# Kernel tuning notes

Measured on AMD Instinct MI355X. Metric: run time of the kernel, lower is better.

Reference implementation:

```python
import jax, jax.numpy as jnp
import numpy as np

IN_FEATURES = 512
NUM_TREES = 512
DEPTH = 5
NLEAF = 2 ** DEPTH
RESPONSE_DIM = 1
BATCH = 2048


def make_path_map():
    # OBLIVIOUS_map from DeTree.InitPathWay: nodes[j] = j (oblivious tree),
    # index 2*node + bit into the flattened [depth, 2] choice tensor.
    path = []
    for no in range(NLEAF):
        b = no
        for j in range(DEPTH):
            path.append(2 * j + (b % 2))
            b //= 2
    return np.asarray(path, dtype=np.int32)  # [NLEAF * DEPTH]


def setup_inputs() -> dict:
    key = jax.random.key(0)
    k1, k2, k3, k4, k5 = jax.random.split(key, 5)
    x = jax.random.normal(k1, (BATCH, IN_FEATURES), dtype=jnp.float32)
    # nn.init.uniform_ on [in_features, num_trees * depth]
    feat_attention = jax.random.uniform(k2, (IN_FEATURES, NUM_TREES * DEPTH), dtype=jnp.float32)
    feature_thresholds = jax.random.normal(k3, (NUM_TREES, DEPTH), dtype=jnp.float32)
    log_temperatures = jax.random.normal(k4, (NUM_TREES, DEPTH), dtype=jnp.float32) * 0.1
    response = jax.random.normal(k5, (NUM_TREES, RESPONSE_DIM, NLEAF), dtype=jnp.float32)
    path_map = jnp.asarray(make_path_map())
    return {"x": x, "feat_attention": feat_attention,
            "feature_thresholds": feature_thresholds,
            "log_temperatures": log_temperatures,
            "response": response, "path_map": path_map}


def reference(x, feat_attention, feature_thresholds, log_temperatures, response, path_map):
    B, F = x.shape
    n, d = feature_thresholds.shape
    # feature gating: softmax over the feature axis (dim=0)
    choice_weight = jax.nn.softmax(feat_attention, axis=0).reshape(F, n, d)
    feature_values = jnp.einsum('bf,fnd->bnd', x, choice_weight)  # [B, n, d]
    # temperature-scaled split logits
    tl = (feature_values - feature_thresholds) * jnp.exp(-log_temperatures)
    logits = jnp.stack([-tl, tl], axis=-1)  # [B, n, d, 2]
    # sparsemoid binary gate
    choice = jnp.clip(0.5 * logits + 0.5, 0.0, 1.0)
    # route through tree paths: gather per-leaf path gates, product along depth
    gate = choice.reshape(B, n, d * 2)[:, :, path_map].reshape(B, n, -1, d)
    bins_prob = jnp.prod(gate, axis=-1)  # [B, n, nLeaf]
    out = jnp.einsum('bnl,ncl->bnc', bins_prob, response)  # [B, n, response_dim]
    return out.reshape(B, -1)  # flatten_output=True
```

## Files before the change

### kernel.cpp

```cpp
#include <hip/hip_runtime.h>
#include <hip/hip_bf16.h>

#define F_DIM 512
#define NT 512
#define DEPTH 5
#define NCOL (NT * DEPTH)
#define BATCH 2048
#define NLEAF 32

typedef __attribute__((ext_vector_type(8))) short bf16x8;
typedef __attribute__((ext_vector_type(4))) float f32x4;

__device__ __forceinline__ void gl2lds16(const void* g, void* l) {
    __builtin_amdgcn_global_load_lds((const __attribute__((address_space(1))) void*)g,
                                     (__attribute__((address_space(3))) void*)l,
                                     16, 0, 0);
}

__global__ __launch_bounds__(256) void softmax_t(const float* __restrict__ fa,
                                                 __hip_bfloat16* __restrict__ Wt) {
    const int l = threadIdx.x & 15;
    const int g = threadIdx.x >> 4;
    const int col = blockIdx.x * 16 + l;
    const int f0 = g * 32;
    __shared__ float red[16][16];

    float s = 0.f;
    for (int i = 0; i < 32; ++i)
        s += __expf(fa[(size_t)(f0 + i) * NCOL + col]);
    red[g][l] = s;
    __syncthreads();

    float S = 0.f;
#pragma unroll
    for (int gg = 0; gg < 16; ++gg) S += red[gg][l];
    const float inv = 1.0f / S;

    __hip_bfloat16* dst = Wt + (size_t)col * F_DIM + f0;
    for (int i = 0; i < 32; i += 4) {
        union { ushort4 u; __hip_bfloat16 h[4]; } pk;
#pragma unroll
        for (int jj = 0; jj < 4; ++jj) {
            float v = __expf(fa[(size_t)(f0 + i + jj) * NCOL + col]) * inv;
            pk.h[jj] = __float2bfloat16(v);
        }
        *(ushort4*)(dst + i) = pk.u;
    }
}

__global__ __launch_bounds__(256) void cast_x(const float* __restrict__ x,
                                              __hip_bfloat16* __restrict__ Xb) {
    const size_t i = (size_t)blockIdx.x * blockDim.x + threadIdx.x;
    const float4 v = ((const float4*)x)[i];
    union { ushort4 u; __hip_bfloat16 h[4]; } pk;
    pk.h[0] = __float2bfloat16(v.x);
    pk.h[1] = __float2bfloat16(v.y);
    pk.h[2] = __float2bfloat16(v.z);
    pk.h[3] = __float2bfloat16(v.w);
    ((ushort4*)Xb)[i] = pk.u;
}

__global__ __launch_bounds__(256) void gemm_bt(const __hip_bfloat16* __restrict__ A,
                                               const __hip_bfloat16* __restrict__ Bt,
                                               float* __restrict__ C) {
    __shared__ __hip_bfloat16 As[128 * 64];
    __shared__ __hip_bfloat16 Bs[128 * 64];

    const int tid = threadIdx.x;
    const int w = tid >> 6;
    const int l = tid & 63;
    const int m0 = blockIdx.y * 128;
    const int n0 = blockIdx.x * 128;
    const int wm = (w & 1) * 64;
    const int wn = (w >> 1) * 64;

    f32x4 acc[4][4] = {};

    const int srow = l >> 3;
    const int schunk = (l & 7) ^ srow;

    for (int kt = 0; kt < 8; ++kt) {
        const int k0 = kt * 64;
#pragma unroll
        for (int q = 0; q < 4; ++q) {
            const int row = q * 32 + w * 8 + srow;
            gl2lds16(A + ((size_t)(m0 + row) * F_DIM + k0 + schunk * 8),
                     As + (q * 32 + w * 8) * 64);
            gl2lds16(Bt + ((size_t)(n0 + row) * F_DIM + k0 + schunk * 8),
                     Bs + (q * 32 + w * 8) * 64);
        }
        __syncthreads();

#pragma unroll
        for (int ks = 0; ks < 2; ++ks) {
            bf16x8 af[4], bfr[4];
            const int cbase = ks * 4 + (l >> 4);
#pragma unroll
            for (int im = 0; im < 4; ++im) {
                const int r = wm + im * 16 + (l & 15);
                af[im] = *(const bf16x8*)(As + r * 64 + ((cbase ^ (r & 7)) * 8));
            }
#pragma unroll
            for (int in = 0; in < 4; ++in) {
                const int r = wn + in * 16 + (l & 15);
                bfr[in] = *(const bf16x8*)(Bs + r * 64 + ((cbase ^ (r & 7)) * 8));
            }
#pragma unroll
            for (int im = 0; im < 4; ++im)
#pragma unroll
                for (int in = 0; in < 4; ++in)
                    acc[im][in] = __builtin_amdgcn_mfma_f32_16x16x32_bf16(
                        af[im], bfr[in], acc[im][in], 0, 0, 0);
        }
        __syncthreads();
    }

    const int cr = (l >> 4) * 4;
    const int cc = l & 15;
#pragma unroll
    for (int im = 0; im < 4; ++im) {
#pragma unroll
        for (int in = 0; in < 4; ++in) {
            float* Cp = C + (size_t)(m0 + wm + im * 16 + cr) * NCOL
                          + (n0 + wn + in * 16 + cc);
#pragma unroll
            for (int r = 0; r < 4; ++r)
                Cp[(size_t)r * NCOL] = acc[im][in][r];
        }
    }
}

__global__ __launch_bounds__(512) void tree_out(const float* __restrict__ fv,
                                                const float* __restrict__ th,
                                                const float* __restrict__ lt,
                                                const float* __restrict__ resp,
                                                float* __restrict__ out) {
    __shared__ float rT[32 * 512];
    const int t = threadIdx.x;

#pragma unroll
    for (int k = 0; k < 32; ++k) {
        const int idx = t + k * 512;
        const int n = idx >> 5, i = idx & 31;
        rT[i * 512 + (n ^ i)] = resp[idx];
    }

    float alpha[DEPTH], beta[DEPTH];
#pragma unroll
    for (int j = 0; j < DEPTH; ++j) {
        const float a = 0.5f * __expf(-lt[t * DEPTH + j]);
        alpha[j] = a;
        beta[j] = 0.5f - th[t * DEPTH + j] * a;
    }
    __syncthreads();

    float r[32];
#pragma unroll
    for (int i = 0; i < 32; ++i) r[i] = rT[i * 512 + (t ^ i)];

    const int b0 = blockIdx.x * 8;
    for (int rr = 0; rr < 8; ++rr) {
        const int b = b0 + rr;
        const float* f = fv + (size_t)b * NCOL + t * DEPTH;
        float c1[DEPTH];
#pragma unroll
        for (int j = 0; j < DEPTH; ++j) {
            const float v = fmaf(alpha[j], f[j], beta[j]);
            c1[j] = fminf(fmaxf(v, 0.f), 1.f);
        }
        float s16[16], s8[8], s4[4], s2[2];
#pragma unroll
        for (int m = 0; m < 16; ++m) s16[m] = fmaf(c1[0], r[2*m+1] - r[2*m], r[2*m]);
#pragma unroll
        for (int m = 0; m < 8; ++m)  s8[m]  = fmaf(c1[1], s16[2*m+1] - s16[2*m], s16[2*m]);
#pragma unroll
        for (int m = 0; m < 4; ++m)  s4[m]  = fmaf(c1[2], s8[2*m+1] - s8[2*m], s8[2*m]);
#pragma unroll
        for (int m = 0; m < 2; ++m)  s2[m]  = fmaf(c1[3], s4[2*m+1] - s4[2*m], s4[2*m]);
        out[(size_t)b * NT + t] = fmaf(c1[4], s2[1] - s2[0], s2[0]);
    }
}

extern "C" void kernel_launch(void* const* d_in, const int* in_sizes, int n_in,
                              void* d_out, int out_size, void* d_ws, size_t ws_size,
                              hipStream_t stream) {
    const float* x    = (const float*)d_in[0];
    const float* fa   = (const float*)d_in[1];
    const float* th   = (const float*)d_in[2];
    const float* lt   = (const float*)d_in[3];
    const float* resp = (const float*)d_in[4];

    char* ws = (char*)d_ws;
    __hip_bfloat16* Wt = (__hip_bfloat16*)(ws);
    __hip_bfloat16* Xb = (__hip_bfloat16*)(ws + (4u << 20));
    float*          fv = (float*)(ws + (8u << 20));
    float* out = (float*)d_out;

    hipLaunchKernelGGL(softmax_t, dim3(NCOL / 16), dim3(256), 0, stream, fa, Wt);
    hipLaunchKernelGGL(cast_x, dim3((BATCH * F_DIM / 4) / 256), dim3(256), 0, stream, x, Xb);
    hipLaunchKernelGGL(gemm_bt, dim3(NCOL / 128, BATCH / 128), dim3(256), 0, stream, Xb, Wt, fv);
    hipLaunchKernelGGL(tree_out, dim3(BATCH / 8), dim3(512), 0, stream, fv, th, lt, resp, out);
}
```

Measured before the change: 97.75 us.

## Fuse tree evaluation into GEMM epilogue and merge prep kernels

The GEMM tile is widened to 160 columns (32 whole trees) so each block holds complete trees. The tree gating and leaf reduction then run in the epilogue from an LDS staging buffer, which removes the fp32 feature_values round trip through global memory and the separate tree kernel. The x cast and the softmax are merged into one launch, and the softmax caches its exponentials in registers instead of reading and exponentiating the input twice. The cost is more accumulators per thread, extra LDS syncs in the epilogue, and a grid of only 16x16 blocks with launch_bounds(256,1).

```diff
diff --git a/kernel.cpp b/kernel.cpp
--- a/kernel.cpp
+++ b/kernel.cpp
@@ -6,7 +6,6 @@
 #define DEPTH 5
 #define NCOL (NT * DEPTH)
 #define BATCH 2048
-#define NLEAF 32
 
 typedef __attribute__((ext_vector_type(8))) short bf16x8;
 typedef __attribute__((ext_vector_type(4))) float f32x4;
@@ -17,17 +16,35 @@
                                      16, 0, 0);
 }
 
-__global__ __launch_bounds__(256) void softmax_t(const float* __restrict__ fa,
-                                                 __hip_bfloat16* __restrict__ Wt) {
+__global__ __launch_bounds__(256) void prep(const float* __restrict__ x,
+                                            const float* __restrict__ fa,
+                                            __hip_bfloat16* __restrict__ Xb,
+                                            __hip_bfloat16* __restrict__ Wt) {
+    if (blockIdx.x < 1024) {
+        const size_t i = (size_t)blockIdx.x * 256 + threadIdx.x;
+        const float4 v = ((const float4*)x)[i];
+        union { ushort4 u; __hip_bfloat16 h[4]; } pk;
+        pk.h[0] = __float2bfloat16(v.x);
+        pk.h[1] = __float2bfloat16(v.y);
+        pk.h[2] = __float2bfloat16(v.z);
+        pk.h[3] = __float2bfloat16(v.w);
+        ((ushort4*)Xb)[i] = pk.u;
+        return;
+    }
+    const int bx = blockIdx.x - 1024;
     const int l = threadIdx.x & 15;
     const int g = threadIdx.x >> 4;
-    const int col = blockIdx.x * 16 + l;
+    const int col = bx * 16 + l;
     const int f0 = g * 32;
     __shared__ float red[16][16];
 
+    float e[32];
     float s = 0.f;
-    for (int i = 0; i < 32; ++i)
-        s += __expf(fa[(size_t)(f0 + i) * NCOL + col]);
+#pragma unroll
+    for (int i = 0; i < 32; ++i) {
+        e[i] = __expf(fa[(size_t)(f0 + i) * NCOL + col]);
+        s += e[i];
+    }
     red[g][l] = s;
     __syncthreads();
 
@@ -37,44 +54,37 @@
     const float inv = 1.0f / S;
 
     __hip_bfloat16* dst = Wt + (size_t)col * F_DIM + f0;
+#pragma unroll
     for (int i = 0; i < 32; i += 4) {
         union { ushort4 u; __hip_bfloat16 h[4]; } pk;
 #pragma unroll
-        for (int jj = 0; jj < 4; ++jj) {
-            float v = __expf(fa[(size_t)(f0 + i + jj) * NCOL + col]) * inv;
-            pk.h[jj] = __float2bfloat16(v);
-        }
+        for (int jj = 0; jj < 4; ++jj)
+            pk.h[jj] = __float2bfloat16(e[i + jj] * inv);
         *(ushort4*)(dst + i) = pk.u;
     }
 }
 
-__global__ __launch_bounds__(256) void cast_x(const float* __restrict__ x,
-                                              __hip_bfloat16* __restrict__ Xb) {
-    const size_t i = (size_t)blockIdx.x * blockDim.x + threadIdx.x;
-    const float4 v = ((const float4*)x)[i];
-    union { ushort4 u; __hip_bfloat16 h[4]; } pk;
-    pk.h[0] = __float2bfloat16(v.x);
-    pk.h[1] = __float2bfloat16(v.y);
-    pk.h[2] = __float2bfloat16(v.z);
-    pk.h[3] = __float2bfloat16(v.w);
-    ((ushort4*)Xb)[i] = pk.u;
-}
-
-__global__ __launch_bounds__(256) void gemm_bt(const __hip_bfloat16* __restrict__ A,
-                                               const __hip_bfloat16* __restrict__ Bt,
-                                               float* __restrict__ C) {
-    __shared__ __hip_bfloat16 As[128 * 64];
-    __shared__ __hip_bfloat16 Bs[128 * 64];
+__global__ __launch_bounds__(256, 1) void gemm_tree(const __hip_bfloat16* __restrict__ A,
+                                                    const __hip_bfloat16* __restrict__ Bt,
+                                                    const float* __restrict__ th,
+                                                    const float* __restrict__ lt,
+                                                    const float* __restrict__ resp,
+                                                    float* __restrict__ out) {
+    __shared__ __align__(16) char smem[36864];
+    __hip_bfloat16* As = (__hip_bfloat16*)smem;
+    __hip_bfloat16* Bs = (__hip_bfloat16*)(smem + 16384);
+    float* E = (float*)smem;
 
     const int tid = threadIdx.x;
     const int w = tid >> 6;
     const int l = tid & 63;
     const int m0 = blockIdx.y * 128;
-    const int n0 = blockIdx.x * 128;
+    const int n0c = blockIdx.x * 160;
+    const int n0t = blockIdx.x * 32;
     const int wm = (w & 1) * 64;
-    const int wn = (w >> 1) * 64;
-
-    f32x4 acc[4][4] = {};
+    const int wn = (w >> 1) * 80;
+
+    f32x4 acc[4][5] = {};
 
     const int srow = l >> 3;
     const int schunk = (l & 7) ^ srow;
@@ -83,101 +93,94 @@
         const int k0 = kt * 64;
 #pragma unroll
         for (int q = 0; q < 4; ++q) {
-            const int row = q * 32 + w * 8 + srow;
-            gl2lds16(A + ((size_t)(m0 + row) * F_DIM + k0 + schunk * 8),
-                     As + (q * 32 + w * 8) * 64);
-            gl2lds16(Bt + ((size_t)(n0 + row) * F_DIM + k0 + schunk * 8),
-                     Bs + (q * 32 + w * 8) * 64);
+            const int g = q * 4 + w;
+            gl2lds16(A + ((size_t)(m0 + g * 8 + srow) * F_DIM + k0 + schunk * 8),
+                     As + g * 8 * 64);
+        }
+#pragma unroll
+        for (int q = 0; q < 5; ++q) {
+            const int g = q * 4 + w;
+            gl2lds16(Bt + ((size_t)(n0c + g * 8 + srow) * F_DIM + k0 + schunk * 8),
+                     Bs + g * 8 * 64);
         }
         __syncthreads();
 
 #pragma unroll
         for (int ks = 0; ks < 2; ++ks) {
-            bf16x8 af[4], bfr[4];
-            const int cbase = ks * 4 + (l >> 4);
+            bf16x8 af[4], bfr[5];
+            const int cb = ks * 4 + (l >> 4);
 #pragma unroll
             for (int im = 0; im < 4; ++im) {
                 const int r = wm + im * 16 + (l & 15);
-                af[im] = *(const bf16x8*)(As + r * 64 + ((cbase ^ (r & 7)) * 8));
-            }
-#pragma unroll
-            for (int in = 0; in < 4; ++in) {
+                af[im] = *(const bf16x8*)(As + r * 64 + ((cb ^ (r & 7)) * 8));
+            }
+#pragma unroll
+            for (int in = 0; in < 5; ++in) {
                 const int r = wn + in * 16 + (l & 15);
-                bfr[in] = *(const bf16x8*)(Bs + r * 64 + ((cbase ^ (r & 7)) * 8));
+                bfr[in] = *(const bf16x8*)(Bs + r * 64 + ((cb ^ (r & 7)) * 8));
             }
 #pragma unroll
             for (int im = 0; im < 4; ++im)
 #pragma unroll
-                for (int in = 0; in < 4; ++in)
+                for (int in = 0; in < 5; ++in)
                     acc[im][in] = __builtin_amdgcn_mfma_f32_16x16x32_bf16(
                         af[im], bfr[in], acc[im][in], 0, 0, 0);
         }
         __syncthreads();
     }
 
-    const int cr = (l >> 4) * 4;
-    const int cc = l & 15;
+    const int tree = tid & 31;
+    const int rg = tid >> 5;
+    const int gt = n0t + tree;
+
+    float al[DEPTH], be[DEPTH];
+#pragma unroll
+    for (int j = 0; j < DEPTH; ++j) {
+        const float a = 0.5f * __expf(-lt[gt * DEPTH + j]);
+        al[j] = a;
+        be[j] = 0.5f - th[gt * DEPTH + j] * a;
+    }
+    float rs[32];
+#pragma unroll
+    for (int i = 0; i < 32; ++i) rs[i] = resp[gt * 32 + i];
+
+    const int PAD = 161;
 #pragma unroll
     for (int im = 0; im < 4; ++im) {
 #pragma unroll
-        for (int in = 0; in < 4; ++in) {
-            float* Cp = C + (size_t)(m0 + wm + im * 16 + cr) * NCOL
-                          + (n0 + wn + in * 16 + cc);
-#pragma unroll
-            for (int r = 0; r < 4; ++r)
-                Cp[(size_t)r * NCOL] = acc[im][in][r];
-        }
-    }
-}
-
-__global__ __launch_bounds__(512) void tree_out(const float* __restrict__ fv,
-                                                const float* __restrict__ th,
-                                                const float* __restrict__ lt,
-                                                const float* __restrict__ resp,
-                                                float* __restrict__ out) {
-    __shared__ float rT[32 * 512];
-    const int t = threadIdx.x;
-
-#pragma unroll
-    for (int k = 0; k < 32; ++k) {
-        const int idx = t + k * 512;
-        const int n = idx >> 5, i = idx & 31;
-        rT[i * 512 + (n ^ i)] = resp[idx];
-    }
-
-    float alpha[DEPTH], beta[DEPTH];
-#pragma unroll
-    for (int j = 0; j < DEPTH; ++j) {
-        const float a = 0.5f * __expf(-lt[t * DEPTH + j]);
-        alpha[j] = a;
-        beta[j] = 0.5f - th[t * DEPTH + j] * a;
-    }
-    __syncthreads();
-
-    float r[32];
-#pragma unroll
-    for (int i = 0; i < 32; ++i) r[i] = rT[i * 512 + (t ^ i)];
-
-    const int b0 = blockIdx.x * 8;
-    for (int rr = 0; rr < 8; ++rr) {
-        const int b = b0 + rr;
-        const float* f = fv + (size_t)b * NCOL + t * DEPTH;
-        float c1[DEPTH];
-#pragma unroll
-        for (int j = 0; j < DEPTH; ++j) {
-            const float v = fmaf(alpha[j], f[j], beta[j]);
-            c1[j] = fminf(fmaxf(v, 0.f), 1.f);
-        }
-        float s16[16], s8[8], s4[4], s2[2];
-#pragma unroll
-        for (int m = 0; m < 16; ++m) s16[m] = fmaf(c1[0], r[2*m+1] - r[2*m], r[2*m]);
-#pragma unroll
-        for (int m = 0; m < 8; ++m)  s8[m]  = fmaf(c1[1], s16[2*m+1] - s16[2*m], s16[2*m]);
-#pragma unroll
-        for (int m = 0; m < 4; ++m)  s4[m]  = fmaf(c1[2], s8[2*m+1] - s8[2*m], s8[2*m]);
-#pragma unroll
-        for (int m = 0; m < 2; ++m)  s2[m]  = fmaf(c1[3], s4[2*m+1] - s4[2*m], s4[2*m]);
-        out[(size_t)b * NT + t] = fmaf(c1[4], s2[1] - s2[0], s2[0]);
+        for (int in = 0; in < 5; ++in) {
+            const int scol = wn + in * 16 + (l & 15);
+#pragma unroll
+            for (int r = 0; r < 4; ++r) {
+                const int sr = (w & 1) * 16 + (l >> 4) * 4 + r;
+                E[sr * PAD + scol] = acc[im][in][r];
+            }
+        }
+        __syncthreads();
+
+#pragma unroll
+        for (int rr = 0; rr < 4; ++rr) {
+            const int s = rg * 4 + rr;
+            const int gb = m0 + ((s < 16) ? (im * 16 + s) : (64 + im * 16 + (s - 16)));
+            const float* f = E + s * PAD + tree * 5;
+            float c1[DEPTH];
+#pragma unroll
+            for (int j = 0; j < DEPTH; ++j) {
+                const float v = fmaf(al[j], f[j], be[j]);
+                c1[j] = fminf(fmaxf(v, 0.f), 1.f);
+            }
+            float s16[16], s8[8], s4[4], s2[2];
+#pragma unroll
+            for (int m = 0; m < 16; ++m) s16[m] = fmaf(c1[0], rs[2*m+1] - rs[2*m], rs[2*m]);
+#pragma unroll
+            for (int m = 0; m < 8; ++m)  s8[m]  = fmaf(c1[1], s16[2*m+1] - s16[2*m], s16[2*m]);
+#pragma unroll
+            for (int m = 0; m < 4; ++m)  s4[m]  = fmaf(c1[2], s8[2*m+1] - s8[2*m], s8[2*m]);
+#pragma unroll
+            for (int m = 0; m < 2; ++m)  s2[m]  = fmaf(c1[3], s4[2*m+1] - s4[2*m], s4[2*m]);
+            out[(size_t)gb * NT + gt] = fmaf(c1[4], s2[1] - s2[0], s2[0]);
+        }
+        __syncthreads();
     }
 }
 
@@ -193,11 +196,9 @@
     char* ws = (char*)d_ws;
     __hip_bfloat16* Wt = (__hip_bfloat16*)(ws);
     __hip_bfloat16* Xb = (__hip_bfloat16*)(ws + (4u << 20));
-    float*          fv = (float*)(ws + (8u << 20));
     float* out = (float*)d_out;
 
-    hipLaunchKernelGGL(softmax_t, dim3(NCOL / 16), dim3(256), 0, stream, fa, Wt);
-    hipLaunchKernelGGL(cast_x, dim3((BATCH * F_DIM / 4) / 256), dim3(256), 0, stream, x, Xb);
-    hipLaunchKernelGGL(gemm_bt, dim3(NCOL / 128, BATCH / 128), dim3(256), 0, stream, Xb, Wt, fv);
-    hipLaunchKernelGGL(tree_out, dim3(BATCH / 8), dim3(512), 0, stream, fv, th, lt, resp, out);
-}
+    hipLaunchKernelGGL(prep, dim3(1024 + 160), dim3(256), 0, stream, x, fa, Xb, Wt);
+    hipLaunchKernelGGL(gemm_tree, dim3(NCOL / 160, BATCH / 128), dim3(256), 0, stream,
+                       Xb, Wt, th, lt, resp, out);
+}
```

Result: faster. 88.11 us (-9.9%).
